# Optimization experiments

Measured on AMD Instinct MI355X. Metric: run time of the kernel, lower is better.

Reference implementation:

```python
import jax, jax.numpy as jnp
import numpy as np

N_HEAD = 8
TOKEN_CODIM = 4   # mixer token codimension; attention uses per-channel tokens (codim 1)
TEMP = 1.0
EPS = 1e-5


def instance_norm(x, w=None, b=None):
    # InstanceNorm2d: normalize each (sample, channel) over spatial dims
    mu = jnp.mean(x, axis=(-2, -1), keepdims=True)
    var = jnp.var(x, axis=(-2, -1), keepdims=True)
    y = (x - mu) * jax.lax.rsqrt(var + EPS)
    if w is not None:
        y = y * w[:, None, None] + b[:, None, None]
    return y


def spectral_conv(x, wr, wi, bias, out_hw):
    # x: (B, Cin, H, W); weight (Cin, Cout, m1, m2) complex; fft_norm='forward'
    B, Cin, H, W = x.shape
    Ho, Wo = out_hw
    w = wr + 1j * wi
    m1, m2 = wr.shape[2], wr.shape[3]
    h = m1 // 2
    xf = jnp.fft.rfft2(x, norm='forward')                  # (B, Cin, H, W//2+1)
    top = jnp.einsum('bixy,ioxy->boxy', xf[:, :, :h, :m2], w[:, :, :h])
    bot = jnp.einsum('bixy,ioxy->boxy', xf[:, :, H - h:, :m2], w[:, :, h:])
    of = jnp.zeros((B, wr.shape[1], Ho, Wo // 2 + 1), dtype=xf.dtype)
    of = of.at[:, :, :h, :m2].set(top)
    of = of.at[:, :, Ho - h:, :m2].set(bot)
    return jnp.fft.irfft2(of, s=(Ho, Wo), norm='forward') + bias[:, None, None]


def fft_resample(x, Ho, Wo):
    # Fourier-truncation resampling (used for the skip branch when the conv rescales)
    B, C, H, W = x.shape
    xf = jnp.fft.rfft2(x, norm='forward')
    h, wc = Ho // 2, Wo // 2 + 1
    of = jnp.zeros((B, C, Ho, wc), dtype=xf.dtype)
    of = of.at[:, :, :h].set(xf[:, :, :h, :wc])
    of = of.at[:, :, Ho - h:].set(xf[:, :, H - h:, :wc])
    return jnp.fft.irfft2(of, s=(Ho, Wo), norm='forward')


def fno_layer(x, wr, wi, bias, sw, sb, out_hw, norm=False, act=False):
    # one FNOBlocks layer: spectral conv (+optional instance norm) + 1x1 linear skip (+act)
    skip = jnp.einsum('bihw,oi->bohw', x, sw) + sb[:, None, None]
    if out_hw != tuple(x.shape[-2:]):
        skip = fft_resample(skip, *out_hw)
    xf = spectral_conv(x, wr, wi, bias, out_hw)
    if norm:
        xf = instance_norm(xf)
    y = xf + skip
    return jax.nn.gelu(y, approximate=False) if act else y


def to_heads(z, b):
    # '(b t) (a d) h w -> b a t (d h w)'
    bt, ad, h, w = z.shape
    t = bt // b
    z = z.reshape(b, t, N_HEAD, ad // N_HEAD, h, w)
    return jnp.transpose(z, (0, 2, 1, 3, 4, 5)).reshape(b, N_HEAD, t, -1)


def setup_inputs():
    key = jax.random.key(0)
    ks = jax.random.split(key, 12)
    b, C, H, W = 2, 128, 128, 128
    f = jax.random.normal
    return dict(
        x=f(ks[0], (b, C, H, W), jnp.float32),
        norm1_w=jnp.ones((1,)), norm1_b=jnp.zeros((1,)),
        kqv_wr=f(ks[1], (3, 1, N_HEAD, 16, 8)) * 0.02,
        kqv_wi=f(ks[2], (3, 1, N_HEAD, 16, 8)) * 0.02,
        kqv_bias=f(ks[3], (3, N_HEAD)) * 0.02,
        kqv_sw=f(ks[4], (3, N_HEAD, 1)) * 0.5,
        kqv_sb=jnp.zeros((3, N_HEAD)),
        p_wr=f(ks[5], (N_HEAD, 1, 32, 16)) * 0.02,
        p_wi=f(ks[6], (N_HEAD, 1, 32, 16)) * 0.02,
        p_bias=jnp.zeros((1,)),
        p_sw=f(ks[7], (1, N_HEAD)) * (1.0 / np.sqrt(N_HEAD)),
        p_sb=jnp.zeros((1,)),
        attn_norm_w=jnp.ones((1,)), attn_norm_b=jnp.zeros((1,)),
        norm2_w=jnp.ones((TOKEN_CODIM,)), norm2_b=jnp.zeros((TOKEN_CODIM,)),
        mix_wr=f(ks[8], (2, TOKEN_CODIM, TOKEN_CODIM, 32, 16)) * 0.02,
        mix_wi=f(ks[9], (2, TOKEN_CODIM, TOKEN_CODIM, 32, 16)) * 0.02,
        mix_bias=jnp.zeros((2, TOKEN_CODIM)),
        mix_sw=f(ks[10], (2, TOKEN_CODIM, TOKEN_CODIM)) * 0.5,
        mix_sb=jnp.zeros((2, TOKEN_CODIM)),
        mon_w=jnp.ones((TOKEN_CODIM,)), mon_b=jnp.zeros((TOKEN_CODIM,)),
    )


def reference(x, norm1_w, norm1_b, kqv_wr, kqv_wi, kqv_bias, kqv_sw, kqv_sb,
              p_wr, p_wi, p_bias, p_sw, p_sb, attn_norm_w, attn_norm_b,
              norm2_w, norm2_b, mix_wr, mix_wi, mix_bias, mix_sw, mix_sb,
              mon_w, mon_b):
    b, C, H, W = x.shape
    tokens = x.reshape(b * C, 1, H, W)                     # per-channel tokens
    tok_n = instance_norm(tokens, norm1_w, norm1_b)        # norm1

    # K, Q downsampled by scale=2; V at full resolution (kqv_modes = n_modes // 2)
    k = fno_layer(tok_n, kqv_wr[0], kqv_wi[0], kqv_bias[0], kqv_sw[0], kqv_sb[0], (H // 2, W // 2))
    q = fno_layer(tok_n, kqv_wr[1], kqv_wi[1], kqv_bias[1], kqv_sw[1], kqv_sb[1], (H // 2, W // 2))
    v = fno_layer(tok_n, kqv_wr[2], kqv_wi[2], kqv_bias[2], kqv_sw[2], kqv_sb[2], (H, W))

    kh, qh, vh = to_heads(k, b), to_heads(q, b), to_heads(v, b)
    scores = jnp.einsum('bati,basi->bats', qh, kh) / (np.float32(np.sqrt(kh.shape[-1])) * TEMP)
    probs = jax.nn.softmax(scores, axis=-1)                # (b, heads, t, t)
    attn = jnp.einsum('bats,basi->bati', probs, vh)        # (b, heads, C, H*W)
    attn = attn.reshape(b, N_HEAD, C, 1, H, W).transpose(0, 2, 1, 3, 4, 5).reshape(b * C, N_HEAD, H, W)

    attn = fno_layer(attn, p_wr, p_wi, p_bias, p_sw, p_sb, (H, W))   # proj heads -> codim 1
    attn = instance_norm(attn + tokens, attn_norm_w, attn_norm_b)

    # regroup channels into mixer tokens of codimension 4
    attn = attn.reshape(b * (C // TOKEN_CODIM), TOKEN_CODIM, H, W)
    h0 = instance_norm(attn, norm2_w, norm2_b)
    h1 = fno_layer(h0, mix_wr[0], mix_wi[0], mix_bias[0], mix_sw[0], mix_sb[0], (H, W), norm=True, act=True)
    h2 = fno_layer(h1, mix_wr[1], mix_wi[1], mix_bias[1], mix_sw[1], mix_sb[1], (H, W), norm=True)
    out = instance_norm(h2, mon_w, mon_b) + attn
    return out.reshape(b, C, H, W)
```

## Files before the change

### kernel.cpp

```cpp
#include <hip/hip_runtime.h>
#include <math.h>


#define NT 2112

__device__ __forceinline__ void blockReduce2(float& a, float& b, float* red){
  const int tid = threadIdx.x, n = blockDim.x;
  red[tid] = a; red[n+tid] = b;
  __syncthreads();
  for(int off=n>>1; off>0; off>>=1){
    if(tid<off){ red[tid]+=red[tid+off]; red[n+tid]+=red[n+tid+off]; }
    __syncthreads();
  }
  a = red[0]; b = red[n];
  __syncthreads();
}

__device__ __forceinline__ float2 cmul_add(float2 acc, float2 w, float2 x){
  acc.x += w.x*x.x - w.y*x.y;
  acc.y += w.x*x.y + w.y*x.x;
  return acc;
}

__global__ void k_tables(float2* __restrict__ CS){
  int a = blockIdx.x, b = threadIdx.x;
  int p = (a*b)&127;
  float t = (float)p * (1.0f/64.0f);
  CS[a*128+b] = make_float2(cospif(t), sinpif(t));
}

__global__ __launch_bounds__(256) void k_instats(
    const float* __restrict__ xin, const float* __restrict__ n1w,
    const float* __restrict__ n1b, float* __restrict__ a1, float* __restrict__ b1)
{
  __shared__ float red[512];
  const int m = blockIdx.x, t = threadIdx.x;
  const float* xp = xin + (size_t)m*16384;
  float s1=0.f, s2=0.f;
  for(int i=t;i<4096;i+=256){
    float4 v = ((const float4*)xp)[i];
    s1 += v.x+v.y+v.z+v.w;
    s2 += v.x*v.x+v.y*v.y+v.z*v.z+v.w*v.w;
  }
  blockReduce2(s1,s2,red);
  if(t==0){
    float mu = s1*(1.0f/16384.0f);
    float var = s2*(1.0f/16384.0f)-mu*mu;
    float a = n1w[0]*rsqrtf(var+1e-5f);
    a1[m] = a; b1[m] = n1b[0] - mu*a;
  }
}

__global__ __launch_bounds__(256) void k_p1(
    const float* __restrict__ xin, float* __restrict__ R1r, float* __restrict__ R1i,
    const float2* __restrict__ CS)
{
  __shared__ float xl[32*129];
  __shared__ float2 csl[4224];
  const int bid = blockIdx.x;
  const int m = bid>>2, yt = bid&3;
  const int t = threadIdx.x;
  for(int i=t;i<4224;i+=256) csl[i] = CS[i];
  {
    const float4* xp4 = (const float4*)(xin + (size_t)m*16384 + yt*4096);
    for(int i4=t;i4<1024;i4+=256){
      float4 v = xp4[i4];
      int y = i4>>5, n = (i4&31)*4;
      xl[y*129+n]=v.x; xl[y*129+n+1]=v.y; xl[y*129+n+2]=v.z; xl[y*129+n+3]=v.w;
    }
  }
  __syncthreads();
  const int yl = t&31, cg = t>>5;
  const int nc = (cg==0)?5:4;
  float ar[5]={0,0,0,0,0}, ai[5]={0,0,0,0,0};
  for(int n=0;n<128;n++){
    float xv = xl[yl*129+n];
    #pragma unroll
    for(int k=0;k<5;k++){
      if(k<nc){
        float2 cs = csl[(cg+8*k)*128+n];
        ar[k] += xv*cs.x;
        ai[k] -= xv*cs.y;
      }
    }
  }
  __syncthreads();
  #pragma unroll
  for(int k=0;k<5;k++){
    if(k<nc){
      int c = cg+8*k;
      xl[yl*33+c] = ar[k];
      xl[1056 + yl*33+c] = ai[k];
    }
  }
  __syncthreads();
  const int gb = m*4224 + yt*1056;
  for(int idx=t; idx<2112; idx+=256){
    if(idx<1056) R1r[gb+idx] = xl[idx];
    else         R1i[gb+idx-1056] = xl[idx];
  }
}

__global__ __launch_bounds__(704) void k_p2(
    const float* __restrict__ R1r, const float* __restrict__ R1i,
    const float2* __restrict__ CS, const float* __restrict__ a1,
    const float* __restrict__ n1b,
    float2* __restrict__ Xt2, float2* __restrict__ Xp)
{
  __shared__ float2 Rl[128*34];
  const int m = blockIdx.x, t = threadIdx.x;
  for(int idx=t; idx<4224; idx+=704){
    int y = idx/33, c = idx - y*33;
    Rl[y*34+c] = make_float2(R1r[m*4224+idx], R1i[m*4224+idx]);
  }
  __syncthreads();
  const float sc = a1[m]*(1.0f/16384.0f);
  const int r = t&63;
  const int ky = (r<32)? r : r+64;
  #pragma unroll
  for(int k=0;k<3;k++){
    int c = (t>>6) + 11*k;
    float ar=0.f, ai=0.f;
    for(int y=0;y<128;y++){
      float2 Rv = Rl[y*34+c];
      float2 cs = CS[128 + ((ky*y)&127)];
      ar += Rv.x*cs.x + Rv.y*cs.y;
      ai += Rv.y*cs.x - Rv.x*cs.y;
    }
    int j = r*33 + c;
    float vr = ar*sc, vi = ai*sc;
    if(j==0){ vr = n1b[0]; vi = 0.f; }
    Xt2[m*NT+j] = make_float2(vr, vi);
    if(c<16 && (r<16 || r>=48)){
      int rp = (r<16)? r : r-32;
      Xp[m*512 + rp*16 + c] = make_float2(vr, vi);
    }
  }
}

__global__ __launch_bounds__(256) void k_build_k(
  const float2* __restrict__ Xt2,
  const float* __restrict__ kqv_wr, const float* __restrict__ kqv_wi,
  const float* __restrict__ kqv_bias, const float* __restrict__ kqv_sw,
  const float* __restrict__ kqv_sb,
  float2* __restrict__ Kc)
{
  __shared__ float2 T[2112];
  __shared__ float2 Ks[2112];
  const int bid = blockIdx.x;
  const int m = bid & 255, o = bid >> 8;
  const int tid = threadIdx.x;
  for(int j=tid;j<2112;j+=256) T[j] = Xt2[m*NT+j];
  __syncthreads();
  const float swK = kqv_sw[o];
  const float swQ = kqv_sw[8+o];
  for(int j=tid;j<2112;j+=256){
    int r = j/33, c = j - r*33;
    float2 X = T[j];
    float2 K = make_float2(swK*X.x, swK*X.y);
    if(c<8){
      int wrow = (r<8)? r : ((r>=56)? r-48 : -1);
      if(wrow>=0)
        K = cmul_add(K, make_float2(kqv_wr[(o*16+wrow)*8+c], kqv_wi[(o*16+wrow)*8+c]), X);
    }
    if(j==0) K.x += kqv_bias[o] + kqv_sb[o];
    Ks[j] = K;
  }
  __syncthreads();
  const size_t ob = ((size_t)(m*8+o))*NT;
  for(int j=tid;j<2112;j+=256){
    int r = j/33, c = j - r*33;
    float2 K = Ks[j];
    float wsc = 128.0f;
    if(c==0 || c==32){
      int pj = ((64-r)&63)*33 + c;
      float2 K2 = Ks[pj];
      K = make_float2(0.5f*(K.x+K2.x), 0.5f*(K.y-K2.y));
      wsc = 64.0f;
    }
    float ar = swQ, ai = 0.f;
    if(c<8){
      int wrow = (r<8)? r : ((r>=56)? r-48 : -1);
      if(wrow>=0){ ar += kqv_wr[((8+o)*16+wrow)*8+c]; ai += kqv_wi[((8+o)*16+wrow)*8+c]; }
    }
    float2 out = make_float2(wsc*(ar*K.x + ai*K.y), wsc*(ar*K.y - ai*K.x));
    if(j==0) out = make_float2(0.f, 0.f);
    Kc[ob+j] = out;
  }
}

__global__ __launch_bounds__(256) void k_scores(
  const float2* __restrict__ Xt2, const float2* __restrict__ Kc,
  float* __restrict__ Pp)
{
  __shared__ float Qs[64*52];
  __shared__ float Ks[64*52];
  const int bid = blockIdx.x;
  const int fq = bid&15, st = (bid>>4)&1, tt = (bid>>5)&1, h = (bid>>6)&7, b = bid>>9;
  const int t = threadIdx.x;
  const int tg = t>>4, sg = t&15;
  const int t0 = tt*64, s0 = st*64;
  const int f2base = fq*132;
  float acc[4][4];
  #pragma unroll
  for(int i=0;i<4;i++)
    #pragma unroll
    for(int j=0;j<4;j++) acc[i][j]=0.f;
  for(int sub=0; sub<6; sub++){
    __syncthreads();
    const int fo = f2base + sub*22;
    for(int idx=t; idx<1408; idx+=256){
      int rl = idx/22, f2 = idx - rl*22;
      float2 q = Xt2[(size_t)(b*128 + t0+rl)*NT + fo + f2];
      ((float2*)(Qs + rl*52))[f2] = q;
      float2 kk = Kc[((size_t)((b*128 + s0+rl)*8+h))*NT + fo + f2];
      ((float2*)(Ks + rl*52))[f2] = kk;
    }
    __syncthreads();
    #pragma unroll
    for(int f4=0; f4<11; f4++){
      float4 qv[4], kv[4];
      #pragma unroll
      for(int i=0;i<4;i++) qv[i] = *(const float4*)&Qs[(tg+16*i)*52 + f4*4];
      #pragma unroll
      for(int j=0;j<4;j++) kv[j] = *(const float4*)&Ks[(sg+16*j)*52 + f4*4];
      #pragma unroll
      for(int i=0;i<4;i++)
        #pragma unroll
        for(int j=0;j<4;j++)
          acc[i][j] += qv[i].x*kv[j].x + qv[i].y*kv[j].y
                     + qv[i].z*kv[j].z + qv[i].w*kv[j].w;
    }
  }
  #pragma unroll
  for(int i=0;i<4;i++){
    int tg2 = t0 + tg + 16*i;
    #pragma unroll
    for(int j=0;j<4;j++){
      int s = s0 + sg + 16*j;
      Pp[(size_t)fq*262144 + ((size_t)((b*8+h)*128+tg2))*128 + s] = acc[i][j];
    }
  }
}

__global__ __launch_bounds__(64) void k_softmax(const float* __restrict__ Pp,
                                                float* __restrict__ P){
  const int row = blockIdx.x, tid = threadIdx.x;
  size_t o = (size_t)row*128;
  float v0=0.f, v1=0.f;
  #pragma unroll
  for(int q=0;q<16;q++){
    v0 += Pp[(size_t)q*262144 + o + tid];
    v1 += Pp[(size_t)q*262144 + o + tid + 64];
  }
  float mx = fmaxf(v0,v1);
  for(int off=32; off; off>>=1) mx = fmaxf(mx, __shfl_xor(mx, off));
  float e0 = expf(v0-mx), e1 = expf(v1-mx);
  float s = e0+e1;
  for(int off=32; off; off>>=1) s += __shfl_xor(s, off);
  float inv = 1.0f/s;
  P[o+tid] = e0*inv; P[o+tid+64] = e1*inv;
}

__global__ __launch_bounds__(256) void k_peff(const float* __restrict__ P,
   const float* __restrict__ p_sw, const float* __restrict__ kqv_sw,
   const float* __restrict__ a1, float* __restrict__ PAT)
{
  const int i = blockIdx.x*256 + threadIdx.x;
  const int b = i>>14, rem = i&16383;
  const int tch = rem>>7, s = rem&127;
  float acc=0.f;
  for(int hh=0; hh<8; hh++){
    float a = p_sw[hh]*kqv_sw[16+hh];
    acc += a * P[(((size_t)(b*8+hh))<<14) + rem];
  }
  PAT[((size_t)(b*128+s))*128 + tch] = acc * a1[b*128+s];
}

__global__ __launch_bounds__(128) void k_pbeta(const float* __restrict__ P,
   const float* __restrict__ p_sw, const float* __restrict__ kqv_sw,
   const float* __restrict__ b1, float* __restrict__ pbeta)
{
  __shared__ float red[128];
  const int bid = blockIdx.x;
  const int b = bid>>7, tch = bid&127;
  const int s = threadIdx.x;
  float acc=0.f;
  for(int hh=0; hh<8; hh++){
    float a = p_sw[hh]*kqv_sw[16+hh];
    acc += a * P[((size_t)((b*8+hh)*128+tch))*128 + s];
  }
  acc *= b1[b*128+s];
  red[s] = acc; __syncthreads();
  for(int off=64; off>0; off>>=1){
    if(s<off) red[s]+=red[s+off];
    __syncthreads();
  }
  if(s==0) pbeta[bid] = red[0];
}

__global__ __launch_bounds__(512) void k_zcorr(
  const float* __restrict__ P, const float2* __restrict__ Xp,
  const float* __restrict__ kqv_wr, const float* __restrict__ kqv_wi,
  const float* __restrict__ kqv_bias, const float* __restrict__ kqv_sw, const float* __restrict__ kqv_sb,
  const float* __restrict__ p_wr, const float* __restrict__ p_wi,
  const float* __restrict__ p_bias, const float* __restrict__ p_sw, const float* __restrict__ p_sb,
  float2* __restrict__ Bc)
{
  __shared__ float4 Xs4[4096];
  __shared__ float Pl[1024];
  const int m = blockIdx.x;
  const int b = m>>7, cix = m&127;
  const int t = threadIdx.x;
  const int j = t;
  for(int idx=t; idx<1024; idx+=512){
    int o = idx>>7, s = idx&127;
    Pl[idx] = P[((size_t)((b*8+o)*128 + cix))*128 + s];
  }
  float2 z[8];
  #pragma unroll
  for(int o=0;o<8;o++) z[o] = make_float2(0.f,0.f);
  const float2* Xs = (const float2*)Xs4;
  for(int st=0; st<8; st++){
    __syncthreads();
    for(int q=t; q<4096; q+=512){
      int sl = q>>8, f4 = q&255;
      Xs4[q] = ((const float4*)(Xp + (size_t)(b*128 + st*16 + sl)*512))[f4];
    }
    __syncthreads();
    for(int sl=0; sl<16; sl++){
      int s = st*16 + sl;
      float2 xv = Xs[sl*512 + j];
      #pragma unroll
      for(int o=0;o<8;o++){
        float p = Pl[o*128+s];
        z[o].x += p*xv.x; z[o].y += p*xv.y;
      }
    }
  }
  __syncthreads();
  float2* Zl = (float2*)Xs4;
  #pragma unroll
  for(int o=0;o<8;o++) Zl[o*512 + j] = z[o];
  __syncthreads();
  {
    int r = j>>4, c = j&15;
    int ky = (r<16)? r : 96+r;
    float accr=0.f, acci=0.f;
    int rp = -1;
    if(c==0){ int kyp = (128-ky)&127; rp = (kyp<16)? kyp : ((kyp>=112)? kyp-96 : -1); }
    for(int o=0;o<8;o++){
      float2 zv = Zl[o*512 + j];
      float cvr=0.f, cvi=0.f;
      bool inV = (c<8) && (ky<8 || ky>=120);
      if(inV){
        int vrow = (ky<8)? ky : 8+(ky-120);
        float wr = kqv_wr[((16+o)*16+vrow)*8+c], wi = kqv_wi[((16+o)*16+vrow)*8+c];
        cvr = wr*zv.x - wi*zv.y; cvi = wr*zv.y + wi*zv.x;
      }
      float ar = cvr, ai = cvi;
      if(c==0){
        float pvr=0.f, pvi=0.f;
        int kyp = (128-ky)&127;
        bool pInV = (kyp<8 || kyp>=120);
        if(pInV && rp>=0){
          int vrow = (kyp<8)? kyp : 8+(kyp-120);
          float2 z2 = Zl[o*512 + rp*16];
          float wr = kqv_wr[((16+o)*16+vrow)*8], wi = kqv_wi[((16+o)*16+vrow)*8];
          pvr = wr*z2.x - wi*z2.y; pvi = wr*z2.y + wi*z2.x;
        }
        ar = 0.5f*(cvr + pvr);
        ai = 0.5f*(cvi - pvi);
      }
      float sv = kqv_sw[16+o];
      float Dv = kqv_bias[16+o] + kqv_sb[16+o];
      float atr = sv*zv.x + ar + ((j==0)? Dv : 0.f);
      float ati = sv*zv.y + ai;
      float psw = p_sw[o];
      accr += psw*ar;  acci += psw*ai;
      float wpr = p_wr[(o*32+r)*16+c], wpi = p_wi[(o*32+r)*16+c];
      accr += wpr*atr - wpi*ati;
      acci += wpr*ati + wpi*atr;
      if(j==0) accr += psw*Dv;
    }
    if(j==0) accr += p_bias[0] + p_sb[0];
    Bc[m*512+j] = make_float2(accr, acci);
  }
}

__global__ __launch_bounds__(256) void k_attn_gemm(
  const float* __restrict__ PAT, const float* __restrict__ xin,
  const float* __restrict__ pbeta, float* __restrict__ y0g)
{
  __shared__ float PAs[32*33];
  __shared__ float Xs[32*256];
  const int bid = blockIdx.x;
  const int b = bid>>8, ct = (bid>>6)&3, pt = bid&63;
  const int t = threadIdx.x;
  const int tc = t>>6, tp = t&63;
  float4 acc[8];
  #pragma unroll
  for(int k=0;k<8;k++) acc[k] = make_float4(0.f,0.f,0.f,0.f);
  for(int sc4=0; sc4<4; sc4++){
    __syncthreads();
    for(int idx=t; idx<1024; idx+=256){
      int sl = idx>>5, cl = idx&31;
      PAs[sl*33+cl] = PAT[((size_t)(b*128 + sc4*32+sl))*128 + ct*32+cl];
    }
    for(int q=t; q<2048; q+=256){
      int sl = q>>6, p4 = q&63;
      ((float4*)Xs)[q] =
        ((const float4*)xin)[((size_t)(b*128 + sc4*32+sl))*4096 + pt*64 + p4];
    }
    __syncthreads();
    for(int sl=0; sl<32; sl++){
      float4 xv = ((const float4*)Xs)[sl*64+tp];
      #pragma unroll
      for(int k=0;k<8;k++){
        float pa = PAs[sl*33 + tc*8+k];
        acc[k].x += pa*xv.x; acc[k].y += pa*xv.y;
        acc[k].z += pa*xv.z; acc[k].w += pa*xv.w;
      }
    }
  }
  #pragma unroll
  for(int k=0;k<8;k++){
    int c = ct*32 + tc*8 + k;
    float pb = pbeta[b*128+c];
    float4 o = acc[k];
    o.x += pb; o.y += pb; o.z += pb; o.w += pb;
    ((float4*)y0g)[((size_t)(b*128+c))*4096 + pt*64 + tp] = o;
  }
}

__global__ __launch_bounds__(1024) void k_epi0(
  const float* __restrict__ y0g, const float* __restrict__ xin,
  const float2* __restrict__ Bc,
  const float2* __restrict__ CS,
  const float* __restrict__ awp, const float* __restrict__ abp,
  const float* __restrict__ n2w, const float* __restrict__ n2b,
  float* __restrict__ attn, float* __restrict__ a2, float* __restrict__ b2,
  float2* __restrict__ Hc)
{
  __shared__ float2 Bcl[512];
  __shared__ float2 V[128*17];
  __shared__ float V2p[128*132];
  __shared__ float red[2048];
  const int m = blockIdx.x, t = threadIdx.x;
  if(t<512) Bcl[t] = Bc[m*512+t];
  __syncthreads();
  #pragma unroll
  for(int k=0;k<2;k++){
    int idx = t + 1024*k;
    int mm = idx>>4, c = idx&15;
    float vr=0.f, vi=0.f;
    for(int r=0;r<32;r++){
      int ky = (r<16)? r : 96+r;
      float2 bc = Bcl[r*16+c];
      float2 cs = CS[128 + ((ky*mm)&127)];
      vr += bc.x*cs.x - bc.y*cs.y;
      vi += bc.x*cs.y + bc.y*cs.x;
    }
    float w = (c==0)?1.0f:2.0f;
    V[mm*17+c] = make_float2(vr*w, vi*w);
  }
  __syncthreads();
  {
    const int n = t&127, mm0 = t>>7;
    float2 csr[16];
    #pragma unroll
    for(int c=0;c<16;c++) csr[c] = CS[c*128+n];
    for(int k=0;k<16;k++){
      int mm = mm0 + 8*k;
      float cv = 0.f;
      #pragma unroll
      for(int c=0;c<16;c++){
        float2 v2 = V[mm*17+c];
        cv += v2.x*csr[c].x - v2.y*csr[c].y;
      }
      V2p[mm*132+n] = cv;
    }
  }
  __syncthreads();
  const float4* x4 = (const float4*)(xin + (size_t)m*16384);
  const float4* g4 = (const float4*)(y0g + (size_t)m*16384);
  float4* V24 = (float4*)V2p;
  float s1=0.f, s2=0.f;
  for(int k=0;k<4;k++){
    int q = t + 1024*k;
    int row = q>>5, c4 = q&31;
    float4 xv = x4[q], gv = g4[q], cc = V24[row*33+c4];
    float4 v;
    v.x = xv.x+gv.x+cc.x; v.y = xv.y+gv.y+cc.y;
    v.z = xv.z+gv.z+cc.z; v.w = xv.w+gv.w+cc.w;
    s1 += v.x+v.y+v.z+v.w;
    s2 += v.x*v.x+v.y*v.y+v.z*v.z+v.w*v.w;
    V24[row*33+c4] = v;
  }
  blockReduce2(s1,s2,red);
  float mu = s1*(1.0f/16384.0f);
  float var = s2*(1.0f/16384.0f)-mu*mu;
  float rs = rsqrtf(var+1e-5f);
  float aw = awp[0], ab = abp[0];
  float4* at4 = (float4*)(attn + (size_t)m*16384);
  for(int k=0;k<4;k++){
    int q = t + 1024*k;
    int row = q>>5, c4 = q&31;
    float4 v = V24[row*33+c4];
    float4 ov;
    ov.x = (v.x-mu)*rs*aw + ab;
    ov.y = (v.y-mu)*rs*aw + ab;
    ov.z = (v.z-mu)*rs*aw + ab;
    ov.w = (v.w-mu)*rs*aw + ab;
    at4[q] = ov;
  }
  float va = aw*aw*var/(var+1e-5f);
  float al = n2w[m&3]*rsqrtf(va+1e-5f);
  if(t==0){ a2[m] = al; b2[m] = n2b[m&3] - ab*al; }
  __syncthreads();
  {
    const int yl = t&31, c = (t>>5)&15, half = t>>9;
    for(int yc=2*half; yc<2*half+2; yc++){
      int y = yc*32+yl;
      float ar=0.f, ai=0.f;
      for(int n=0;n<128;n++){
        float zv = V2p[y*132+n];
        float2 cs = CS[c*128+n];
        ar += zv*cs.x; ai -= zv*cs.y;
      }
      V[y*17+c] = make_float2(ar, ai);
    }
  }
  __syncthreads();
  if(t<512){
    const float scl = al*rs*aw*(1.0f/16384.0f);
    int idx = t;
    int r = idx>>4, c = idx&15;
    int ky = (r<16)? r : 96+r;
    float hr=0.f, hi=0.f;
    for(int y=0;y<128;y++){
      float2 Rv = V[y*17+c];
      float2 cs = CS[128 + ((ky*y)&127)];
      hr += Rv.x*cs.x + Rv.y*cs.y;
      hi += Rv.y*cs.x - Rv.x*cs.y;
    }
    float2 o = make_float2(hr*scl, hi*scl);
    if(idx==0) o = make_float2(n2b[m&3], 0.f);
    Hc[m*512+idx] = o;
  }
}

__global__ __launch_bounds__(1024) void k_mixinv(
  const float2* __restrict__ Hcin, const float* __restrict__ inmaps,
  const float* __restrict__ a2, const float* __restrict__ b2,
  const float* __restrict__ wr0, const float* __restrict__ wi0,
  const float* __restrict__ msw, const float* __restrict__ msb,
  const float2* __restrict__ CS, const int dogelu,
  float2* __restrict__ HcOut,
  const float* __restrict__ addsrc, const float* __restrict__ mw,
  const float* __restrict__ mbv,
  float* __restrict__ outp)
{
  __shared__ float2 Hcl[2048];
  __shared__ float2 Sl[512];
  __shared__ float2 V[128*17];
  __shared__ float V2p[128*132];
  __shared__ float red[2048];
  const int mb = blockIdx.x;
  const int g = mb&63, o = mb>>6;
  const int mmap = g*4+o;
  const int t = threadIdx.x;
  float cw[4]; float cb = msb[o];
  #pragma unroll
  for(int i=0;i<4;i++){
    float al = a2 ? a2[g*4+i] : 1.0f;
    float be = b2 ? b2[g*4+i] : 0.0f;
    float sw = msw[o*4+i];
    cw[i] = sw*al; cb += sw*be;
  }
  #pragma unroll
  for(int k=0;k<2;k++){
    int idx = t + 1024*k;
    Hcl[idx] = Hcin[(size_t)(g*4 + (idx>>9))*512 + (idx&511)];
  }
  __syncthreads();
  if(t<512){
    int j = t, r = j>>4, c = j&15;
    float ar=0.f, ai=0.f;
    for(int i2=0;i2<4;i2++){
      float2 h = Hcl[i2*512 + j];
      float wr = wr0[((i2*4+o)*32+r)*16+c], wi = wi0[((i2*4+o)*32+r)*16+c];
      ar += wr*h.x - wi*h.y; ai += wr*h.y + wi*h.x;
    }
    Sl[j] = make_float2(ar, ai);
  }
  __syncthreads();
  float vs=0.f, dummy=0.f;
  if(t<512){
    int c = t&15;
    if(c>=1) vs = 2.0f*(Sl[t].x*Sl[t].x + Sl[t].y*Sl[t].y);
  }
  if(t<32){
    int ky = (t<16)? (t+1) : (96+t);
    float ar=0.f, ai=0.f;
    if(ky<16){ ar=Sl[ky*16].x; ai=Sl[ky*16].y; }
    else if(ky>=112){ int r=ky-96; ar=Sl[r*16].x; ai=Sl[r*16].y; }
    int kyp = 128-ky;
    float br2=0.f, bi2=0.f;
    if(kyp<16){ br2=Sl[kyp*16].x; bi2=Sl[kyp*16].y; }
    else if(kyp>=112){ int r=kyp-96; br2=Sl[r*16].x; bi2=Sl[r*16].y; }
    float pr = 0.5f*(ar+br2), pi = 0.5f*(ai-bi2);
    vs += pr*pr + pi*pi;
  }
  blockReduce2(vs, dummy, red);
  float rs2 = rsqrtf(vs + 1e-5f);
  if(t<512){
    float2 s = Sl[t];
    Sl[t] = (t==0)? make_float2(0.f,0.f) : make_float2(s.x*rs2, s.y*rs2);
  }
  __syncthreads();
  #pragma unroll
  for(int k=0;k<2;k++){
    int idx = t + 1024*k;
    int mm = idx>>4, c = idx&15;
    float vr=0.f, vi=0.f;
    for(int r=0;r<32;r++){
      int ky = (r<16)? r : 96+r;
      float2 bc = Sl[r*16+c];
      float2 cs = CS[128 + ((ky*mm)&127)];
      vr += bc.x*cs.x - bc.y*cs.y;
      vi += bc.x*cs.y + bc.y*cs.x;
    }
    float w = (c==0)?1.0f:2.0f;
    V[mm*17+c] = make_float2(vr*w, vi*w);
  }
  __syncthreads();
  {
    const int n = t&127, mm0 = t>>7;
    float2 csr[16];
    #pragma unroll
    for(int c=0;c<16;c++) csr[c] = CS[c*128+n];
    for(int k=0;k<16;k++){
      int mm = mm0 + 8*k;
      float cv = 0.f;
      #pragma unroll
      for(int c=0;c<16;c++){
        float2 v2 = V[mm*17+c];
        cv += v2.x*csr[c].x - v2.y*csr[c].y;
      }
      V2p[mm*132+n] = cv;
    }
  }
  __syncthreads();
  const float4* in4 = (const float4*)(inmaps + (size_t)(g*4)*16384);
  float4* V24 = (float4*)V2p;
  float4* o4 = (float4*)(outp + (size_t)mmap*16384);
  float s1=0.f, s2=0.f;
  for(int k=0;k<4;k++){
    int q = t + 1024*k;
    int row = q>>5, c4 = q&31;
    float4 v0 = in4[q], v1 = in4[4096+q], v2 = in4[8192+q], v3 = in4[12288+q];
    float4 cc = V24[row*33+c4];
    float4 ov;
    ov.x = cb + cw[0]*v0.x + cw[1]*v1.x + cw[2]*v2.x + cw[3]*v3.x + cc.x;
    ov.y = cb + cw[0]*v0.y + cw[1]*v1.y + cw[2]*v2.y + cw[3]*v3.y + cc.y;
    ov.z = cb + cw[0]*v0.z + cw[1]*v1.z + cw[2]*v2.z + cw[3]*v3.z + cc.z;
    ov.w = cb + cw[0]*v0.w + cw[1]*v1.w + cw[2]*v2.w + cw[3]*v3.w + cc.w;
    if(dogelu){
      ov.x = 0.5f*ov.x*(1.0f+erff(ov.x*0.70710678118f));
      ov.y = 0.5f*ov.y*(1.0f+erff(ov.y*0.70710678118f));
      ov.z = 0.5f*ov.z*(1.0f+erff(ov.z*0.70710678118f));
      ov.w = 0.5f*ov.w*(1.0f+erff(ov.w*0.70710678118f));
    }
    if(addsrc){
      s1 += ov.x+ov.y+ov.z+ov.w;
      s2 += ov.x*ov.x+ov.y*ov.y+ov.z*ov.z+ov.w*ov.w;
      V24[row*33+c4] = ov;
    } else {
      o4[q] = ov;
      if(HcOut) V24[row*33+c4] = ov;
    }
  }
  if(addsrc){
    blockReduce2(s1,s2,red);
    float mu = s1*(1.0f/16384.0f);
    float var = s2*(1.0f/16384.0f)-mu*mu;
    float rs = rsqrtf(var+1e-5f);
    float w = mw[o], b = mbv[o];
    const float4* a4 = (const float4*)(addsrc + (size_t)mmap*16384);
    for(int k=0;k<4;k++){
      int q = t + 1024*k;
      int row = q>>5, c4 = q&31;
      float4 v = V24[row*33+c4], av = a4[q];
      float4 ov;
      ov.x = (v.x-mu)*rs*w + b + av.x;
      ov.y = (v.y-mu)*rs*w + b + av.y;
      ov.z = (v.z-mu)*rs*w + b + av.z;
      ov.w = (v.w-mu)*rs*w + b + av.w;
      o4[q] = ov;
    }
  }
  if(HcOut){
    __syncthreads();
    {
      const int yl = t&31, c = (t>>5)&15, half = t>>9;
      for(int yc=2*half; yc<2*half+2; yc++){
        int y = yc*32+yl;
        float ar=0.f, ai=0.f;
        for(int n=0;n<128;n++){
          float zv = V2p[y*132+n];
          float2 cs = CS[c*128+n];
          ar += zv*cs.x; ai -= zv*cs.y;
        }
        V[y*17+c] = make_float2(ar, ai);
      }
    }
    __syncthreads();
    if(t<512){
      int idx = t;
      int r = idx>>4, c = idx&15;
      int ky = (r<16)? r : 96+r;
      float hr=0.f, hi=0.f;
      for(int y=0;y<128;y++){
        float2 Rv = V[y*17+c];
        float2 cs = CS[128 + ((ky*y)&127)];
        hr += Rv.x*cs.x + Rv.y*cs.y;
        hi += Rv.y*cs.x - Rv.x*cs.y;
      }
      HcOut[mmap*512+idx] = make_float2(hr*(1.0f/16384.0f), hi*(1.0f/16384.0f));
    }
  }
}

extern "C" void kernel_launch(void* const* d_in, const int* in_sizes, int n_in,
                              void* d_out, int out_size, void* d_ws, size_t ws_size,
                              hipStream_t stream)
{
  const float* x        = (const float*)d_in[0];
  const float* norm1_w  = (const float*)d_in[1];
  const float* norm1_b  = (const float*)d_in[2];
  const float* kqv_wr   = (const float*)d_in[3];
  const float* kqv_wi   = (const float*)d_in[4];
  const float* kqv_bias = (const float*)d_in[5];
  const float* kqv_sw   = (const float*)d_in[6];
  const float* kqv_sb   = (const float*)d_in[7];
  const float* p_wr     = (const float*)d_in[8];
  const float* p_wi     = (const float*)d_in[9];
  const float* p_bias   = (const float*)d_in[10];
  const float* p_sw     = (const float*)d_in[11];
  const float* p_sb     = (const float*)d_in[12];
  const float* attn_norm_w = (const float*)d_in[13];
  const float* attn_norm_b = (const float*)d_in[14];
  const float* norm2_w  = (const float*)d_in[15];
  const float* norm2_b  = (const float*)d_in[16];
  const float* mix_wr   = (const float*)d_in[17];
  const float* mix_wi   = (const float*)d_in[18];
  const float* mix_sw   = (const float*)d_in[20];
  const float* mix_sb   = (const float*)d_in[21];
  const float* mon_w    = (const float*)d_in[22];
  const float* mon_b    = (const float*)d_in[23];
  float* out = (float*)d_out;

  const size_t NEED = (size_t)26576128 * sizeof(float);
  if(ws_size < NEED) return;

  float* ws = (float*)d_ws;
  size_t off = 0;
  float2* CS  = (float2*)(ws + off); off += 32768;
  float* a1   = ws + off; off += 256;
  float* b1   = ws + off; off += 256;
  float* a2   = ws + off; off += 256;
  float* b2   = ws + off; off += 256;
  float* pbeta= ws + off; off += 256;
  float2* Xt2 = (float2*)(ws + off); off += 1081344;
  float* pool = ws + off; off += 17301504;
  float* P    = ws + off; off += 262144;
  float* PAT  = ws + off; off += 32768;
  float2* Xp  = (float2*)(ws + off); off += 262144;
  float* Zc_unused = ws + off; off += 2097152;
  float2* Bc  = (float2*)(ws + off); off += 262144;
  float* attn = ws + off; off += 4194304;
  float2* Hc  = (float2*)(ws + off); off += 524288;
  float2* Hc2 = (float2*)(ws + off); off += 524288;
  (void)Zc_unused;

  float* Pp   = attn;

  float2* Kc = (float2*)pool;
  float* R1r = pool + 8650752;
  float* R1i = pool + 8650752 + 1081344;
  float* y0g = pool;
  float* h1  = pool + 4325376;

  k_tables<<<dim3(128), dim3(128), 0, stream>>>(CS);
  k_instats<<<dim3(256), dim3(256), 0, stream>>>(x, norm1_w, norm1_b, a1, b1);
  k_p1<<<dim3(1024), dim3(256), 0, stream>>>(x, R1r, R1i, CS);
  k_p2<<<dim3(256), dim3(704), 0, stream>>>(R1r, R1i, CS, a1, norm1_b, Xt2, Xp);
  k_build_k<<<dim3(2048), dim3(256), 0, stream>>>(Xt2, kqv_wr, kqv_wi, kqv_bias,
                                                  kqv_sw, kqv_sb, Kc);
  k_scores<<<dim3(1024), dim3(256), 0, stream>>>(Xt2, Kc, Pp);
  k_softmax<<<dim3(2048), dim3(64), 0, stream>>>(Pp, P);
  k_peff<<<dim3(128), dim3(256), 0, stream>>>(P, p_sw, kqv_sw, a1, PAT);
  k_pbeta<<<dim3(256), dim3(128), 0, stream>>>(P, p_sw, kqv_sw, b1, pbeta);
  k_zcorr<<<dim3(256), dim3(512), 0, stream>>>(P, Xp, kqv_wr, kqv_wi, kqv_bias, kqv_sw, kqv_sb,
                                               p_wr, p_wi, p_bias, p_sw, p_sb, Bc);
  k_attn_gemm<<<dim3(512), dim3(256), 0, stream>>>(PAT, x, pbeta, y0g);
  k_epi0<<<dim3(256), dim3(1024), 0, stream>>>(y0g, x, Bc, CS, attn_norm_w, attn_norm_b,
                                               norm2_w, norm2_b, attn, a2, b2, Hc);
  k_mixinv<<<dim3(256), dim3(1024), 0, stream>>>(Hc, attn, a2, b2, mix_wr, mix_wi,
                                                 mix_sw, mix_sb, CS, 1,
                                                 Hc2, (const float*)nullptr,
                                                 (const float*)nullptr, (const float*)nullptr, h1);
  k_mixinv<<<dim3(256), dim3(1024), 0, stream>>>(Hc2, h1, (const float*)nullptr, (const float*)nullptr,
                                                 mix_wr+8192, mix_wi+8192, mix_sw+16, mix_sb+4, CS, 0,
                                                 (float2*)nullptr, attn, mon_w, mon_b, out);
}
```

Measured before the change: 376.1 us.

## Split attention scores into shared Gram term plus sparse per-head low-mode correction

Per-head key spectra are rewritten as a scaled copy of the shared token spectrum plus a correction that is nonzero only on the 129 retained Fourier modes. The full-length score GEMM is now done once per batch, head-independent, and a small per-head GEMM over the support handles the corrections. Softmax combines the two with the per-head scale. This cuts the dominant per-head key build and score traffic by about the head count, at the cost of two extra kernels and a more delicate decomposition, including the bias and conjugate-symmetric columns.

```diff
diff --git a/kernel.cpp b/kernel.cpp
--- a/kernel.cpp
+++ b/kernel.cpp
@@ -3,6 +3,7 @@
 
 
 #define NT 2112
+#define NSUP 132
 
 __device__ __forceinline__ void blockReduce2(float& a, float& b, float* red){
   const int tid = threadIdx.x, n = blockDim.x;
@@ -20,6 +21,11 @@
   acc.x += w.x*x.x - w.y*x.y;
   acc.y += w.x*x.y + w.y*x.x;
   return acc;
+}
+
+__device__ __forceinline__ void sup_rc(int u, int& r, int& c){
+  if(u<112){ c = (u>>4)+1; int k = u&15; r = (k<8)? k : 48+k; }
+  else { int v = u-112; c = 0; r = (v<9)? v : 47+v; }
 }
 
 __global__ void k_tables(float2* __restrict__ CS){
@@ -138,82 +144,96 @@
   }
 }
 
-__global__ __launch_bounds__(256) void k_build_k(
+__global__ __launch_bounds__(256) void k_build_w(
+  const float2* __restrict__ Xt2, float2* __restrict__ Xw)
+{
+  __shared__ float2 T[2112];
+  const int m = blockIdx.x, t = threadIdx.x;
+  for(int j=t;j<2112;j+=256) T[j] = Xt2[m*NT+j];
+  __syncthreads();
+  for(int j=t;j<2112;j+=256){
+    int r = j/33, c = j - r*33;
+    float2 X = T[j];
+    float wsc = 128.0f;
+    if(c==0 || c==32){
+      int pj = ((64-r)&63)*33 + c;
+      float2 X2 = T[pj];
+      X = make_float2(0.5f*(X.x+X2.x), 0.5f*(X.y-X2.y));
+      wsc = 64.0f;
+    }
+    Xw[m*NT+j] = make_float2(X.x*wsc, X.y*wsc);
+  }
+}
+
+__global__ __launch_bounds__(256) void k_build_d(
   const float2* __restrict__ Xt2,
   const float* __restrict__ kqv_wr, const float* __restrict__ kqv_wi,
   const float* __restrict__ kqv_bias, const float* __restrict__ kqv_sw,
   const float* __restrict__ kqv_sb,
-  float2* __restrict__ Kc)
-{
-  __shared__ float2 T[2112];
-  __shared__ float2 Ks[2112];
+  float2* __restrict__ DL)
+{
   const int bid = blockIdx.x;
-  const int m = bid & 255, o = bid >> 8;
-  const int tid = threadIdx.x;
-  for(int j=tid;j<2112;j+=256) T[j] = Xt2[m*NT+j];
-  __syncthreads();
-  const float swK = kqv_sw[o];
-  const float swQ = kqv_sw[8+o];
-  for(int j=tid;j<2112;j+=256){
-    int r = j/33, c = j - r*33;
-    float2 X = T[j];
-    float2 K = make_float2(swK*X.x, swK*X.y);
-    if(c<8){
-      int wrow = (r<8)? r : ((r>=56)? r-48 : -1);
-      if(wrow>=0)
-        K = cmul_add(K, make_float2(kqv_wr[(o*16+wrow)*8+c], kqv_wi[(o*16+wrow)*8+c]), X);
-    }
-    if(j==0) K.x += kqv_bias[o] + kqv_sb[o];
-    Ks[j] = K;
-  }
-  __syncthreads();
-  const size_t ob = ((size_t)(m*8+o))*NT;
-  for(int j=tid;j<2112;j+=256){
-    int r = j/33, c = j - r*33;
-    float2 K = Ks[j];
-    float wsc = 128.0f;
-    if(c==0 || c==32){
-      int pj = ((64-r)&63)*33 + c;
-      float2 K2 = Ks[pj];
-      K = make_float2(0.5f*(K.x+K2.x), 0.5f*(K.y-K2.y));
-      wsc = 64.0f;
-    }
+  const int m = bid & 255, h = bid >> 8;
+  const int u = threadIdx.x;
+  if(u >= NSUP) return;
+  float2 dv = make_float2(0.f, 0.f);
+  if(u < 129){
+    const float swK = kqv_sw[h], swQ = kqv_sw[8+h];
+    const float biasK = kqv_bias[h] + kqv_sb[h];
+    int r, c; sup_rc(u, r, c);
+    float2 X = Xt2[m*NT + r*33 + c];
+    float2 K1 = make_float2(swK*X.x, swK*X.y);
+    int wr_ = (r<8)? r : ((r>=56)? r-48 : -1);
+    if(wr_>=0)
+      K1 = cmul_add(K1, make_float2(kqv_wr[(h*16+wr_)*8+c], kqv_wi[(h*16+wr_)*8+c]), X);
+    if(r==0 && c==0) K1.x += biasK;
+    float2 PK, PX;
+    if(c==0){
+      int rp = (64-r)&63;
+      float2 Xp_ = Xt2[m*NT + rp*33];
+      float2 K1p = make_float2(swK*Xp_.x, swK*Xp_.y);
+      int wrp = (rp<8)? rp : ((rp>=56)? rp-48 : -1);
+      if(wrp>=0)
+        K1p = cmul_add(K1p, make_float2(kqv_wr[(h*16+wrp)*8], kqv_wi[(h*16+wrp)*8]), Xp_);
+      if(rp==0) K1p.x += biasK;
+      PK = make_float2(0.5f*(K1.x+K1p.x), 0.5f*(K1.y-K1p.y));
+      PX = make_float2(0.5f*(X.x+Xp_.x), 0.5f*(X.y-Xp_.y));
+    } else { PK = K1; PX = X; }
     float ar = swQ, ai = 0.f;
-    if(c<8){
-      int wrow = (r<8)? r : ((r>=56)? r-48 : -1);
-      if(wrow>=0){ ar += kqv_wr[((8+o)*16+wrow)*8+c]; ai += kqv_wi[((8+o)*16+wrow)*8+c]; }
-    }
-    float2 out = make_float2(wsc*(ar*K.x + ai*K.y), wsc*(ar*K.y - ai*K.x));
-    if(j==0) out = make_float2(0.f, 0.f);
-    Kc[ob+j] = out;
-  }
-}
-
-__global__ __launch_bounds__(256) void k_scores(
-  const float2* __restrict__ Xt2, const float2* __restrict__ Kc,
-  float* __restrict__ Pp)
+    if(wr_>=0){ ar += kqv_wr[((8+h)*16+wr_)*8+c]; ai += kqv_wi[((8+h)*16+wr_)*8+c]; }
+    float wsc = (c==0)? 64.0f : 128.0f;
+    float2 Kpp = make_float2(wsc*(ar*PK.x + ai*PK.y), wsc*(ar*PK.y - ai*PK.x));
+    float scq = swQ*swK*wsc;
+    dv = make_float2(Kpp.x - scq*PX.x, Kpp.y - scq*PX.y);
+  }
+  DL[(size_t)(m*8+h)*NSUP + u] = dv;
+}
+
+__global__ __launch_bounds__(256) void k_scoresG(
+  const float2* __restrict__ Xt2, const float2* __restrict__ Xw,
+  float* __restrict__ Gp)
 {
   __shared__ float Qs[64*52];
   __shared__ float Ks[64*52];
   const int bid = blockIdx.x;
-  const int fq = bid&15, st = (bid>>4)&1, tt = (bid>>5)&1, h = (bid>>6)&7, b = bid>>9;
+  const int fq = bid&31, st = (bid>>5)&1, tt = (bid>>6)&1, b = bid>>7;
   const int t = threadIdx.x;
   const int tg = t>>4, sg = t&15;
   const int t0 = tt*64, s0 = st*64;
-  const int f2base = fq*132;
+  const int fb = fq*66;
   float acc[4][4];
   #pragma unroll
   for(int i=0;i<4;i++)
     #pragma unroll
     for(int j=0;j<4;j++) acc[i][j]=0.f;
-  for(int sub=0; sub<6; sub++){
-    __syncthreads();
-    const int fo = f2base + sub*22;
+  for(int sub=0; sub<3; sub++){
+    __syncthreads();
+    const int fo = fb + sub*22;
     for(int idx=t; idx<1408; idx+=256){
       int rl = idx/22, f2 = idx - rl*22;
       float2 q = Xt2[(size_t)(b*128 + t0+rl)*NT + fo + f2];
       ((float2*)(Qs + rl*52))[f2] = q;
-      float2 kk = Kc[((size_t)((b*128 + s0+rl)*8+h))*NT + fo + f2];
+      float2 kk = Xw[(size_t)(b*128 + s0+rl)*NT + fo + f2];
       ((float2*)(Ks + rl*52))[f2] = kk;
     }
     __syncthreads();
@@ -238,21 +258,69 @@
     #pragma unroll
     for(int j=0;j<4;j++){
       int s = s0 + sg + 16*j;
-      Pp[(size_t)fq*262144 + ((size_t)((b*8+h)*128+tg2))*128 + s] = acc[i][j];
-    }
-  }
-}
-
-__global__ __launch_bounds__(64) void k_softmax(const float* __restrict__ Pp,
+      Gp[(size_t)(fq*2+b)*16384 + tg2*128 + s] = acc[i][j];
+    }
+  }
+}
+
+__global__ __launch_bounds__(256) void k_scoresD(
+  const float2* __restrict__ Xt2, const float2* __restrict__ DL,
+  float* __restrict__ Dout)
+{
+  __shared__ float XT[32*268];
+  __shared__ float DS[32*268];
+  const int bid = blockIdx.x;
+  const int b = bid>>7, h = (bid>>4)&7, tt4 = (bid>>2)&3, st4 = bid&3;
+  const int t0 = tt4*32, s0 = st4*32;
+  const int t = threadIdx.x;
+  for(int idx=t; idx<32*NSUP; idx+=256){
+    int row = idx/NSUP, u = idx - row*NSUP;
+    float2 v = make_float2(0.f,0.f);
+    if(u<129){
+      int r, c; sup_rc(u, r, c);
+      v = Xt2[(size_t)(b*128 + t0+row)*NT + r*33 + c];
+    }
+    XT[row*268 + 2*u] = v.x; XT[row*268 + 2*u+1] = v.y;
+    float2 d = DL[(size_t)((b*128 + s0+row)*8 + h)*NSUP + u];
+    DS[row*268 + 2*u] = d.x; DS[row*268 + 2*u+1] = d.y;
+  }
+  __syncthreads();
+  const int tq = t>>4, sq = t&15;
+  float acc[2][2] = {{0.f,0.f},{0.f,0.f}};
+  for(int f4=0; f4<66; f4++){
+    float4 xa0 = *(const float4*)&XT[(tq*2+0)*268 + f4*4];
+    float4 xa1 = *(const float4*)&XT[(tq*2+1)*268 + f4*4];
+    float4 da0 = *(const float4*)&DS[(sq*2+0)*268 + f4*4];
+    float4 da1 = *(const float4*)&DS[(sq*2+1)*268 + f4*4];
+    acc[0][0] += xa0.x*da0.x + xa0.y*da0.y + xa0.z*da0.z + xa0.w*da0.w;
+    acc[0][1] += xa0.x*da1.x + xa0.y*da1.y + xa0.z*da1.z + xa0.w*da1.w;
+    acc[1][0] += xa1.x*da0.x + xa1.y*da0.y + xa1.z*da0.z + xa1.w*da0.w;
+    acc[1][1] += xa1.x*da1.x + xa1.y*da1.y + xa1.z*da1.z + xa1.w*da1.w;
+  }
+  #pragma unroll
+  for(int i=0;i<2;i++)
+    #pragma unroll
+    for(int j=0;j<2;j++)
+      Dout[(size_t)((b*8+h)*128 + t0+tq*2+i)*128 + s0+sq*2+j] = acc[i][j];
+}
+
+__global__ __launch_bounds__(64) void k_softmax(const float* __restrict__ Gp,
+                                                const float* __restrict__ Dout,
+                                                const float* __restrict__ kqv_sw,
                                                 float* __restrict__ P){
   const int row = blockIdx.x, tid = threadIdx.x;
+  const int b = row>>10, h = (row>>7)&7, trow = row&127;
+  const float sch = kqv_sw[8+h]*kqv_sw[h];
+  const size_t gbase = (size_t)b*16384 + trow*128;
+  float v0=0.f, v1=0.f;
+  #pragma unroll
+  for(int q=0;q<32;q++){
+    v0 += Gp[(size_t)(q*2)*16384 + gbase + tid];
+    v1 += Gp[(size_t)(q*2)*16384 + gbase + tid + 64];
+  }
   size_t o = (size_t)row*128;
-  float v0=0.f, v1=0.f;
-  #pragma unroll
-  for(int q=0;q<16;q++){
-    v0 += Pp[(size_t)q*262144 + o + tid];
-    v1 += Pp[(size_t)q*262144 + o + tid + 64];
-  }
+  v0 = sch*v0 + Dout[o+tid];
+  v1 = sch*v1 + Dout[o+tid+64];
   float mx = fmaxf(v0,v1);
   for(int off=32; off; off>>=1) mx = fmaxf(mx, __shfl_xor(mx, off));
   float e0 = expf(v0-mx), e1 = expf(v1-mx);
@@ -777,16 +845,17 @@
   float* P    = ws + off; off += 262144;
   float* PAT  = ws + off; off += 32768;
   float2* Xp  = (float2*)(ws + off); off += 262144;
-  float* Zc_unused = ws + off; off += 2097152;
+  float* Zslab= ws + off; off += 2097152;
   float2* Bc  = (float2*)(ws + off); off += 262144;
   float* attn = ws + off; off += 4194304;
   float2* Hc  = (float2*)(ws + off); off += 524288;
   float2* Hc2 = (float2*)(ws + off); off += 524288;
-  (void)Zc_unused;
-
-  float* Pp   = attn;
-
-  float2* Kc = (float2*)pool;
+
+  float2* DL  = (float2*)Zslab;
+  float* Gp   = attn;
+  float* Dout = attn + 1048576;
+
+  float2* Xw = (float2*)pool;
   float* R1r = pool + 8650752;
   float* R1i = pool + 8650752 + 1081344;
   float* y0g = pool;
@@ -796,10 +865,12 @@
   k_instats<<<dim3(256), dim3(256), 0, stream>>>(x, norm1_w, norm1_b, a1, b1);
   k_p1<<<dim3(1024), dim3(256), 0, stream>>>(x, R1r, R1i, CS);
   k_p2<<<dim3(256), dim3(704), 0, stream>>>(R1r, R1i, CS, a1, norm1_b, Xt2, Xp);
-  k_build_k<<<dim3(2048), dim3(256), 0, stream>>>(Xt2, kqv_wr, kqv_wi, kqv_bias,
-                                                  kqv_sw, kqv_sb, Kc);
-  k_scores<<<dim3(1024), dim3(256), 0, stream>>>(Xt2, Kc, Pp);
-  k_softmax<<<dim3(2048), dim3(64), 0, stream>>>(Pp, P);
+  k_build_w<<<dim3(256), dim3(256), 0, stream>>>(Xt2, Xw);
+  k_build_d<<<dim3(2048), dim3(256), 0, stream>>>(Xt2, kqv_wr, kqv_wi, kqv_bias,
+                                                  kqv_sw, kqv_sb, DL);
+  k_scoresG<<<dim3(256), dim3(256), 0, stream>>>(Xt2, Xw, Gp);
+  k_scoresD<<<dim3(256), dim3(256), 0, stream>>>(Xt2, DL, Dout);
+  k_softmax<<<dim3(2048), dim3(64), 0, stream>>>(Gp, Dout, kqv_sw, P);
   k_peff<<<dim3(128), dim3(256), 0, stream>>>(P, p_sw, kqv_sw, a1, PAT);
   k_pbeta<<<dim3(256), dim3(128), 0, stream>>>(P, p_sw, kqv_sw, b1, pbeta);
   k_zcorr<<<dim3(256), dim3(512), 0, stream>>>(P, Xp, kqv_wr, kqv_wi, kqv_bias, kqv_sw, kqv_sb,
```

Result: faster. 339.0 us (-9.9%).
